# Kernel tuning notes

Hardware: AMD Instinct MI355X
Metric: run time of the kernel (lower is better)

## Reference

```python
import jax, jax.numpy as jnp
import numpy as np

B, C, H, W = 32, 128, 56, 56
CMAX, OUT, KS, K = 128, 256, 3, 4
HID = 64  # attn_fc hidden width


def setup_inputs() -> dict:
    key = jax.random.key(0)
    ks = jax.random.split(key, 6)
    x = jax.random.normal(ks[0], (B, C, H, W), dtype=jnp.float32)
    weight_bank = jax.random.normal(ks[1], (K, OUT, CMAX, KS, KS), dtype=jnp.float32)
    fc1_w = jax.random.normal(ks[2], (HID, CMAX), dtype=jnp.float32) * (1.0 / np.sqrt(CMAX))
    fc1_b = jnp.zeros((HID,), dtype=jnp.float32)
    fc2_w = jax.random.normal(ks[3], (K, HID), dtype=jnp.float32) * (1.0 / np.sqrt(HID))
    fc2_b = jnp.zeros((K,), dtype=jnp.float32)
    return {"x": x, "weight_bank": weight_bank, "fc1_w": fc1_w, "fc1_b": fc1_b,
            "fc2_w": fc2_w, "fc2_b": fc2_b}


def reference(x, weight_bank, fc1_w, fc1_b, fc2_w, fc2_b):
    b, c, h, w = x.shape
    # AdaptiveAvgPool2d(1) on zero-channel-padded input -> mean over HW, pad channel dim
    pooled = jnp.mean(x, axis=(2, 3))                       # [B, C]
    pooled = jnp.pad(pooled, ((0, 0), (0, CMAX - c)))       # [B, CMAX]
    hdn = jax.nn.relu(pooled @ fc1_w.T + fc1_b)             # [B, 64]
    attn = jax.nn.softmax(hdn @ fc2_w.T + fc2_b, axis=-1)   # [B, K]
    # per-sample kernel synthesis
    weight = jnp.einsum('bk,kocij->bocij', attn, weight_bank[:, :, :c])  # [B,O,C,k,k]
    # single grouped conv instead of B separate conv launches
    lhs = x.reshape(1, b * c, h, w)
    rhs = weight.reshape(b * OUT, c, KS, KS)
    p = KS // 2
    out = jax.lax.conv_general_dilated(
        lhs, rhs, window_strides=(1, 1), padding=[(p, p), (p, p)],
        feature_group_count=b,
        dimension_numbers=('NCHW', 'OIHW', 'NCHW'))
    return out.reshape(b, OUT, h, w)
```

## Files before the change

### kernel.cpp

```cpp
#include <hip/hip_runtime.h>
#include <hip/hip_bf16.h>

#define B_    32
#define C_    128
#define H_    56
#define W_    56
#define OUT_  256
#define K_    4
#define HID_  64
#define HW_   (H_*W_)
#define KV_   (C_*9)
#define PH_   58
#define PW_   58
#define PP_   (PH_*PW_)

typedef __attribute__((ext_vector_type(8))) short short8_t;
typedef __attribute__((ext_vector_type(4))) float float4_t;

typedef __hip_bfloat16 bf16;

__device__ __forceinline__ short f2bf(float v) {
    union { bf16 h; short s; } u; u.h = __float2bfloat16(v); return u.s;
}

typedef __attribute__((address_space(1))) const unsigned int* gas_t;
typedef __attribute__((address_space(3))) unsigned int* las_t;

__device__ __forceinline__ void gl_lds16(const short* g, short* l) {
    __builtin_amdgcn_global_load_lds((gas_t)(const void*)g, (las_t)(void*)l, 16, 0, 0);
}

__global__ __launch_bounds__(256) void dc_xt(const float* __restrict__ x,
                                             short* __restrict__ xTp,
                                             float* __restrict__ pooled) {
    int b = blockIdx.y, n0 = blockIdx.x * 128;
    __shared__ short t[C_][130];
    int lane = threadIdx.x & 63;
    for (int i = threadIdx.x; i < C_*128; i += 256) {
        int c = i >> 7, nn = i & 127;
        int pp = n0 + nn;
        int py = pp / PW_, px = pp - py*PW_;
        bool valid = (pp < PP_) & (py >= 1) & (py <= H_) & (px >= 1) & (px <= W_);
        float v = valid ? x[((size_t)b*C_ + c)*HW_ + (py-1)*W_ + (px-1)] : 0.f;
        t[c][nn] = f2bf(v);
        float s = v;
        for (int off = 32; off > 0; off >>= 1) s += __shfl_down(s, off, 64);
        if (lane == 0 && s != 0.f) atomicAdd(&pooled[b*C_ + c], s);
    }
    __syncthreads();
    for (int i = threadIdx.x; i < 64*128; i += 256) {
        int nn = i >> 6, c2 = (i & 63) * 2;
        int pp = n0 + nn;
        if (pp < PP_) {
            union { unsigned short u[2]; unsigned v; } pk;
            pk.u[0] = (unsigned short)t[c2][nn];
            pk.u[1] = (unsigned short)t[c2+1][nn];
            *(unsigned*)&xTp[((size_t)b*PP_ + pp)*C_ + c2] = pk.v;
        }
    }
}

__global__ __launch_bounds__(64) void dc_attn(const float* __restrict__ pooled,
                                              const float* __restrict__ fc1w,
                                              const float* __restrict__ fc1b,
                                              const float* __restrict__ fc2w,
                                              const float* __restrict__ fc2b,
                                              float* __restrict__ attn) {
    int b = blockIdx.x, h = threadIdx.x;
    __shared__ float pl[C_];
    __shared__ float hdn[HID_];
    __shared__ float logit[K_];
    pl[h]      = pooled[b*C_ + h]      * (1.0f / HW_);
    pl[h + 64] = pooled[b*C_ + 64 + h] * (1.0f / HW_);
    __syncthreads();
    float s = fc1b[h];
    #pragma unroll 8
    for (int c = 0; c < C_; ++c) s += pl[c] * fc1w[h*C_ + c];
    hdn[h] = fmaxf(s, 0.f);
    __syncthreads();
    if (h < K_) {
        float t = fc2b[h];
        #pragma unroll 8
        for (int j = 0; j < HID_; ++j) t += hdn[j] * fc2w[h*HID_ + j];
        logit[h] = t;
    }
    __syncthreads();
    if (h == 0) {
        float m = fmaxf(fmaxf(logit[0], logit[1]), fmaxf(logit[2], logit[3]));
        float e0 = __expf(logit[0]-m), e1 = __expf(logit[1]-m);
        float e2 = __expf(logit[2]-m), e3 = __expf(logit[3]-m);
        float inv = 1.0f / (e0+e1+e2+e3);
        attn[b*K_+0]=e0*inv; attn[b*K_+1]=e1*inv;
        attn[b*K_+2]=e2*inv; attn[b*K_+3]=e3*inv;
    }
}

__global__ __launch_bounds__(256) void dc_wsynth(const float* __restrict__ bank,
                                                 const float* __restrict__ attn,
                                                 bf16* __restrict__ Ws) {
    int o = blockIdx.x;
    int b0 = blockIdx.y * 8;
    __shared__ float wb[4*KV_];
    for (int i = threadIdx.x; i < 4*KV_; i += 256) {
        int kk = i / KV_, r = i - kk*KV_;
        wb[i] = bank[((size_t)kk*OUT_ + o)*KV_ + r];
    }
    __syncthreads();
    for (int bi = 0; bi < 8; ++bi) {
        int b = b0 + bi;
        float a0 = attn[b*K_+0], a1 = attn[b*K_+1];
        float a2 = attn[b*K_+2], a3 = attn[b*K_+3];
        unsigned* dst = (unsigned*)&Ws[((size_t)b*OUT_ + o)*KV_];
        for (int ii = threadIdx.x; ii < KV_/2; ii += 256) {
            int i0 = 2*ii;
            int tap0 = i0 >> 7, c0 = i0 & 127;
            int i1 = i0 + 1;
            int tap1 = i1 >> 7, c1 = i1 & 127;
            float v0 = a0*wb[c0*9+tap0] + a1*wb[KV_+c0*9+tap0]
                     + a2*wb[2*KV_+c0*9+tap0] + a3*wb[3*KV_+c0*9+tap0];
            float v1 = a0*wb[c1*9+tap1] + a1*wb[KV_+c1*9+tap1]
                     + a2*wb[2*KV_+c1*9+tap1] + a3*wb[3*KV_+c1*9+tap1];
            union { unsigned short u[2]; unsigned v; } pk;
            pk.u[0] = (unsigned short)f2bf(v0);
            pk.u[1] = (unsigned short)f2bf(v1);
            dst[ii] = pk.v;
        }
    }
}

__global__ __launch_bounds__(256) void dc_gemm(const short* __restrict__ Ws,
                                               const short* __restrict__ xTp,
                                               float* __restrict__ out) {
    const int nwg = 25 * 2 * B_;
    const int cpx = nwg >> 3;
    int orig = blockIdx.x;
    int swz  = (orig & 7) * cpx + (orig >> 3);
    const int bx  = swz % 25;
    const int byz = swz / 25;
    const int by  = byz & 1;
    const int b   = byz >> 1;

    const int m0 = by * 128;
    const int n0 = bx * 128;
    const int tid  = threadIdx.x;
    const int lane = tid & 63;
    const int wv   = tid >> 6;
    const int wm   = wv & 1, wn = wv >> 1;
    const int l16  = lane & 15, quad = lane >> 4;

    __shared__ short lA[2][8192];
    __shared__ short lB[2][8192];

    const short* aG[4];
    const short* bG[4];
    int segOff[4];
    #pragma unroll
    for (int j = 0; j < 4; ++j) {
        int t = 4*wv + j;
        int row = (t >> 1) * 16 + l16;
        int kq  = t & 1;
        aG[j] = Ws + ((size_t)b*OUT_ + m0 + row)*KV_ + kq*32 + quad*8;
        int n = n0 + row;
        int idc = min(n, HW_ - 1);
        int y = idc / W_, xx2 = idc - y * W_;
        int pbc = (y + 1) * PW_ + (xx2 + 1);
        bG[j] = xTp + ((size_t)b*PP_ + pbc)*C_ + kq*32 + quad*8;
        segOff[j] = t * 512;
    }

    int nidx[4];
    #pragma unroll
    for (int ni = 0; ni < 4; ++ni)
        nidx[ni] = n0 + wn*64 + ni*16 + l16;

    float4_t acc[4][4];
    #pragma unroll
    for (int mi = 0; mi < 4; ++mi)
        #pragma unroll
        for (int ni = 0; ni < 4; ++ni)
            acc[mi][ni] = (float4_t){0.f, 0.f, 0.f, 0.f};

    auto stage = [&](int s, int buf) {
        int tap = s >> 1;
        int ty = tap / 3, tx = tap - 3*ty;
        int doff = ((ty - 1) * PW_ + (tx - 1)) * C_;
        int ka = s * 64;
        int cb = (s & 1) * 64;
        #pragma unroll
        for (int j = 0; j < 4; ++j) {
            gl_lds16(aG[j] + ka,        lA[buf] + segOff[j]);
            gl_lds16(bG[j] + doff + cb, lB[buf] + segOff[j]);
        }
    };

    auto compute = [&](int buf) {
        #pragma unroll
        for (int kq = 0; kq < 2; ++kq) {
            short8_t af[4], bf[4];
            #pragma unroll
            for (int mi = 0; mi < 4; ++mi)
                af[mi] = *(const short8_t*)(lA[buf] + ((wm*4+mi)*2 + kq)*512 + lane*8);
            #pragma unroll
            for (int ni = 0; ni < 4; ++ni)
                bf[ni] = *(const short8_t*)(lB[buf] + ((wn*4+ni)*2 + kq)*512 + lane*8);
            #pragma unroll
            for (int mi = 0; mi < 4; ++mi)
                #pragma unroll
                for (int ni = 0; ni < 4; ++ni)
                    acc[mi][ni] = __builtin_amdgcn_mfma_f32_16x16x32_bf16(
                        af[mi], bf[ni], acc[mi][ni], 0, 0, 0);
        }
    };

    stage(0, 0);
    __syncthreads();
    int cur = 0;
    for (int s = 0; s < 18; ++s) {
        if (s < 17) stage(s + 1, cur ^ 1);
        compute(cur);
        __syncthreads();
        cur ^= 1;
    }

    const size_t obase = (size_t)b * OUT_ * HW_;
    #pragma unroll
    for (int mi = 0; mi < 4; ++mi) {
        int m = m0 + wm*64 + mi*16 + quad*4;
        #pragma unroll
        for (int ni = 0; ni < 4; ++ni) {
            int n = nidx[ni];
            if (n < HW_) {
                float* op = out + obase + (size_t)m * HW_ + n;
                #pragma unroll
                for (int r = 0; r < 4; ++r)
                    op[(size_t)r * HW_] = acc[mi][ni][r];
            }
        }
    }
}

extern "C" void kernel_launch(void* const* d_in, const int* in_sizes, int n_in,
                              void* d_out, int out_size, void* d_ws, size_t ws_size,
                              hipStream_t stream) {
    const float* x    = (const float*)d_in[0];
    const float* bank = (const float*)d_in[1];
    const float* fc1w = (const float*)d_in[2];
    const float* fc1b = (const float*)d_in[3];
    const float* fc2w = (const float*)d_in[4];
    const float* fc2b = (const float*)d_in[5];
    float* out = (float*)d_out;

    char* ws = (char*)d_ws;
    float* pooled = (float*)ws;
    float* attn   = (float*)(ws + 16*1024);
    bf16*  Ws     = (bf16*) (ws + 32*1024);
    short* xTp    = (short*)(ws + 32*1024 + 18874368);

    hipMemsetAsync(pooled, 0, B_*C_*sizeof(float), stream);
    dc_xt    <<<dim3(27, B_), 256, 0, stream>>>(x, xTp, pooled);
    dc_attn  <<<B_,     64, 0, stream>>>(pooled, fc1w, fc1b, fc2w, fc2b, attn);
    dc_wsynth<<<dim3(OUT_, 4), 256, 0, stream>>>(bank, attn, Ws);
    dc_gemm  <<<dim3(1600), 256, 0, stream>>>((const short*)Ws, xTp, out);
}
```

Before: 384.7 us.

## Drop LDS staging in conv GEMM; load MFMA fragments directly from global

Replaces the double-buffered global_load_lds staging and per-stage barriers with direct per-wave global loads of A and B fragments for every tap and k-chunk, fully unrolled. Launch bounds now request 3 blocks per SM. The aim is to remove LDS traffic and synchronisation overhead and rely on L1/L2 for reuse across waves. The cost is that each wave re-reads operand data that other waves in the block share, which raises global and cache traffic. Without explicit prefetch, load latency may no longer overlap with compute.

```diff
diff --git a/kernel.cpp b/kernel.cpp
--- a/kernel.cpp
+++ b/kernel.cpp
@@ -21,13 +21,6 @@
 
 __device__ __forceinline__ short f2bf(float v) {
     union { bf16 h; short s; } u; u.h = __float2bfloat16(v); return u.s;
-}
-
-typedef __attribute__((address_space(1))) const unsigned int* gas_t;
-typedef __attribute__((address_space(3))) unsigned int* las_t;
-
-__device__ __forceinline__ void gl_lds16(const short* g, short* l) {
-    __builtin_amdgcn_global_load_lds((gas_t)(const void*)g, (las_t)(void*)l, 16, 0, 0);
 }
 
 __global__ __launch_bounds__(256) void dc_xt(const float* __restrict__ x,
@@ -128,9 +121,9 @@
     }
 }
 
-__global__ __launch_bounds__(256) void dc_gemm(const short* __restrict__ Ws,
-                                               const short* __restrict__ xTp,
-                                               float* __restrict__ out) {
+__global__ __launch_bounds__(256, 3) void dc_gemm(const short* __restrict__ Ws,
+                                                  const short* __restrict__ xTp,
+                                                  float* __restrict__ out) {
     const int nwg = 25 * 2 * B_;
     const int cpx = nwg >> 3;
     int orig = blockIdx.x;
@@ -148,30 +141,23 @@
     const int wm   = wv & 1, wn = wv >> 1;
     const int l16  = lane & 15, quad = lane >> 4;
 
-    __shared__ short lA[2][8192];
-    __shared__ short lB[2][8192];
-
-    const short* aG[4];
-    const short* bG[4];
-    int segOff[4];
-    #pragma unroll
-    for (int j = 0; j < 4; ++j) {
-        int t = 4*wv + j;
-        int row = (t >> 1) * 16 + l16;
-        int kq  = t & 1;
-        aG[j] = Ws + ((size_t)b*OUT_ + m0 + row)*KV_ + kq*32 + quad*8;
-        int n = n0 + row;
+    const short* aB[4];
+    #pragma unroll
+    for (int mi = 0; mi < 4; ++mi) {
+        int row = m0 + wm*64 + mi*16 + l16;
+        aB[mi] = Ws + ((size_t)b*OUT_ + row)*KV_ + quad*8;
+    }
+    const short* bB[4];
+    int nidx[4];
+    #pragma unroll
+    for (int ni = 0; ni < 4; ++ni) {
+        int n = n0 + wn*64 + ni*16 + l16;
+        nidx[ni] = n;
         int idc = min(n, HW_ - 1);
-        int y = idc / W_, xx2 = idc - y * W_;
-        int pbc = (y + 1) * PW_ + (xx2 + 1);
-        bG[j] = xTp + ((size_t)b*PP_ + pbc)*C_ + kq*32 + quad*8;
-        segOff[j] = t * 512;
-    }
-
-    int nidx[4];
-    #pragma unroll
-    for (int ni = 0; ni < 4; ++ni)
-        nidx[ni] = n0 + wn*64 + ni*16 + l16;
+        int y = idc / W_, xx = idc - y*W_;
+        int pbc = (y + 1)*PW_ + (xx + 1);
+        bB[ni] = xTp + ((size_t)b*PP_ + pbc)*C_ + quad*8;
+    }
 
     float4_t acc[4][4];
     #pragma unroll
@@ -180,29 +166,19 @@
         for (int ni = 0; ni < 4; ++ni)
             acc[mi][ni] = (float4_t){0.f, 0.f, 0.f, 0.f};
 
-    auto stage = [&](int s, int buf) {
-        int tap = s >> 1;
-        int ty = tap / 3, tx = tap - 3*ty;
-        int doff = ((ty - 1) * PW_ + (tx - 1)) * C_;
-        int ka = s * 64;
-        int cb = (s & 1) * 64;
+    #pragma unroll
+    for (int tap = 0; tap < 9; ++tap) {
+        const int ty = tap / 3, tx = tap - 3*ty;
+        const int doff = ((ty - 1)*PW_ + (tx - 1)) * C_;
         #pragma unroll
-        for (int j = 0; j < 4; ++j) {
-            gl_lds16(aG[j] + ka,        lA[buf] + segOff[j]);
-            gl_lds16(bG[j] + doff + cb, lB[buf] + segOff[j]);
-        }
-    };
-
-    auto compute = [&](int buf) {
-        #pragma unroll
-        for (int kq = 0; kq < 2; ++kq) {
+        for (int kq = 0; kq < 4; ++kq) {
             short8_t af[4], bf[4];
             #pragma unroll
             for (int mi = 0; mi < 4; ++mi)
-                af[mi] = *(const short8_t*)(lA[buf] + ((wm*4+mi)*2 + kq)*512 + lane*8);
+                af[mi] = *(const short8_t*)(aB[mi] + tap*128 + kq*32);
             #pragma unroll
             for (int ni = 0; ni < 4; ++ni)
-                bf[ni] = *(const short8_t*)(lB[buf] + ((wn*4+ni)*2 + kq)*512 + lane*8);
+                bf[ni] = *(const short8_t*)(bB[ni] + doff + kq*32);
             #pragma unroll
             for (int mi = 0; mi < 4; ++mi)
                 #pragma unroll
@@ -210,16 +186,6 @@
                     acc[mi][ni] = __builtin_amdgcn_mfma_f32_16x16x32_bf16(
                         af[mi], bf[ni], acc[mi][ni], 0, 0, 0);
         }
-    };
-
-    stage(0, 0);
-    __syncthreads();
-    int cur = 0;
-    for (int s = 0; s < 18; ++s) {
-        if (s < 17) stage(s + 1, cur ^ 1);
-        compute(cur);
-        __syncthreads();
-        cur ^= 1;
     }
 
     const size_t obase = (size_t)b * OUT_ * HW_;
```

Measured after the change: 468.9 us. +21.9%, slower.
